# Optimization experiments

Hardware: AMD Instinct MI355X
Metric: run time of the kernel (lower is better)

The kernel has to match this reference:

```python
import jax, jax.numpy as jnp
import numpy as np

NUM_GROUPS = 32
EPS = 1e-5


def group_norm(x, scale, bias):
    # x: [B, C, L], normalize per (group, batch) over (C//G, L)
    B, C, L = x.shape
    G = NUM_GROUPS
    xg = x.reshape(B, G, C // G, L)
    mean = xg.mean(axis=(2, 3), keepdims=True)
    var = xg.var(axis=(2, 3), keepdims=True)
    xg = (xg - mean) * jax.lax.rsqrt(var + EPS)
    h = xg.reshape(B, C, L)
    return h * scale[None, :, None] + bias[None, :, None]


def setup_inputs() -> dict:
    key = jax.random.key(0)
    ks = jax.random.split(key, 8)
    B, C, L = 8, 512, 2048
    s = 1.0 / np.sqrt(C)
    return {
        "x": jax.random.normal(ks[0], (B, C, L), jnp.float32),
        "gn_scale": jnp.ones((C,), jnp.float32),
        "gn_bias": jnp.zeros((C,), jnp.float32),
        "wq": jax.random.normal(ks[1], (C, C), jnp.float32) * s,
        "bq": jnp.zeros((C,), jnp.float32),
        "wk": jax.random.normal(ks[2], (C, C), jnp.float32) * s,
        "bk": jnp.zeros((C,), jnp.float32),
        "wv": jax.random.normal(ks[3], (C, C), jnp.float32) * s,
        "bv": jnp.zeros((C,), jnp.float32),
        "wo": jax.random.normal(ks[4], (C, C), jnp.float32) * s,
        "bo": jnp.zeros((C,), jnp.float32),
    }


def reference(x, gn_scale, gn_bias, wq, bq, wk, bk, wv, bv, wo, bo):
    B, C, L = x.shape
    h = group_norm(x, gn_scale, gn_bias)  # [B, C, L]
    # 1x1 conv == per-position linear; produce [B, L, C] directly
    q = jnp.einsum('oc,bcl->blo', wq, h) + bq
    k = jnp.einsum('oc,bcl->blo', wk, h) + bk
    v = jnp.einsum('oc,bcl->blo', wv, h) + bv
    scale = jnp.asarray(C, x.dtype) ** -0.5
    w = jnp.einsum('bqc,bkc->bqk', q, k) * scale  # [B, L, L]
    w = jax.nn.softmax(w, axis=-1)
    a = jnp.einsum('bqk,bkc->bqc', w, v)  # [B, L, C]
    out = jnp.einsum('oc,blc->bol', wo, a) + bo[None, :, None]  # [B, C, L]
    return x + out
```

## Files before the change

### kernel.cpp

```cpp
#include <hip/hip_runtime.h>

typedef __attribute__((ext_vector_type(8))) _Float16 half8;
typedef __attribute__((ext_vector_type(4))) float floatx4;

#define AS1 __attribute__((address_space(1)))
#define AS3 __attribute__((address_space(3)))

__device__ __forceinline__ void async_load16(const void* g, void* l) {
  __builtin_amdgcn_global_load_lds((AS1 void*)(unsigned long long)g,
                                   (AS3 void*)(unsigned long long)l, 16, 0, 0);
}

__global__ __launch_bounds__(256) void gn_stats(const float* __restrict__ x,
                                                float* __restrict__ stats) {
  const int bg = blockIdx.x;
  const float4* p4 = (const float4*)(x + (long long)bg * 32768);
  const int t = threadIdx.x;
  float s = 0.f, ss = 0.f;
  for (int i = t; i < 8192; i += 256) {
    float4 v = p4[i];
    s += v.x + v.y + v.z + v.w;
    ss += v.x * v.x + v.y * v.y + v.z * v.z + v.w * v.w;
  }
#pragma unroll
  for (int off = 32; off; off >>= 1) { s += __shfl_down(s, off); ss += __shfl_down(ss, off); }
  __shared__ float rs[4], rss[4];
  if ((t & 63) == 0) { rs[t >> 6] = s; rss[t >> 6] = ss; }
  __syncthreads();
  if (t == 0) {
    s = rs[0] + rs[1] + rs[2] + rs[3];
    ss = rss[0] + rss[1] + rss[2] + rss[3];
    float mean = s * (1.f / 32768.f);
    float var = ss * (1.f / 32768.f) - mean * mean;
    stats[bg] = mean;
    stats[256 + bg] = rsqrtf(var + 1e-5f);
  }
}

__global__ __launch_bounds__(256) void gn_apply(const float* __restrict__ x,
                                                const float* __restrict__ stats,
                                                const float* __restrict__ gsc,
                                                const float* __restrict__ gbi,
                                                _Float16* __restrict__ ht) {
  __shared__ float tile[64][65];
  const int b = blockIdx.z, c0 = blockIdx.y * 64, l0 = blockIdx.x * 64;
  const int t = threadIdx.x, tr = t >> 6, tc = t & 63;
  const float* xb = x + ((long long)b * 512 + c0) * 2048 + l0;
#pragma unroll
  for (int p = 0; p < 16; ++p) {
    int row = tr + p * 4;
    tile[row][tc] = xb[(long long)row * 2048 + tc];
  }
  __syncthreads();
  const int c = c0 + tc;
  const int bg = b * 32 + (c >> 4);
  const float mean = stats[bg], rstd = stats[256 + bg];
  const float sc = gsc[c] * rstd;
  const float off = gbi[c] - mean * sc;
  _Float16* hb = ht + ((long long)b * 2048 + l0) * 512 + c0;
#pragma unroll
  for (int p = 0; p < 16; ++p) {
    int l = tr + p * 4;
    hb[(long long)l * 512 + tc] = (_Float16)(tile[tc][l] * sc + off);
  }
}

__global__ __launch_bounds__(256) void cast_w(const float* __restrict__ w0, const float* __restrict__ w1,
                                              const float* __restrict__ w2, const float* __restrict__ w3,
                                              const float* __restrict__ bq, const float* __restrict__ bk,
                                              _Float16* __restrict__ outw, float* __restrict__ bqk) {
  const long long i = (long long)blockIdx.x * 256 + threadIdx.x;
  if (blockIdx.x < 4096) {
    const int m = (int)(i >> 18);
    const int r = (int)(i & 262143);
    const float* w = (m == 0) ? w0 : (m == 1) ? w1 : (m == 2) ? w2 : w3;
    outw[i] = (_Float16)w[r];
  } else {
    const int j = (int)(i - 4096LL * 256);
    bqk[j] = (j < 512) ? bq[j] : bk[j - 512];
  }
}

template <int BIAS_MODE , int OUT_TYPE , bool RESIDUAL>
__global__ __launch_bounds__(256) void gemm_bt(
    const _Float16* __restrict__ A, long long sA, int lda,
    const _Float16* __restrict__ Bt, long long sB, int ldb,
    void* __restrict__ Cv, long long sC, int ldc,
    const float* __restrict__ bias,
    const float* __restrict__ resid, long long sR,
    float alpha, int K) {
  __shared__ __align__(16) _Float16 lsa[128 * 64];
  __shared__ __align__(16) _Float16 lsb[128 * 64];
  const int tid = threadIdx.x;
  const int wave = tid >> 6, lane = tid & 63;
  const int bz = blockIdx.x;
  const int m0 = blockIdx.y * 128, n0 = blockIdx.z * 128;
  A += (long long)bz * sA;
  Bt += (long long)bz * sB;

  const bool isA = (wave < 2);
  const _Float16* gsrc = isA ? A : Bt;
  const int ld = isA ? lda : ldb;
  const int rbase = (wave & 1) * 64;
  const int t0 = isA ? m0 : n0;
  _Float16* lbase = (isA ? lsa : lsb) + rbase * 64;
  const int grow = t0 + rbase + (lane >> 3);
  const int gcol = ((lane & 7) ^ ((lane >> 3) & 7)) * 8;

  floatx4 acc[4][4] = {};
  const int mw = (wave >> 1) * 64, nw = (wave & 1) * 64;
  const int fm = lane & 15;
  const int quad = lane >> 4;

  for (int k0 = 0; k0 < K; k0 += 64) {
    __syncthreads();
    const _Float16* g = gsrc + (long long)grow * ld + k0 + gcol;
#pragma unroll
    for (int s = 0; s < 8; ++s)
      async_load16(g + (long long)s * 8 * ld, lbase + s * 512);
    __syncthreads();
#pragma unroll
    for (int kk = 0; kk < 2; ++kk) {
      const int ca = quad + 4 * kk;
      const int cs = (ca ^ (fm & 7)) * 8;
      half8 af[4], bfr[4];
#pragma unroll
      for (int i = 0; i < 4; ++i) af[i] = *(const half8*)&lsa[(mw + 16 * i + fm) * 64 + cs];
#pragma unroll
      for (int j = 0; j < 4; ++j) bfr[j] = *(const half8*)&lsb[(nw + 16 * j + fm) * 64 + cs];
#pragma unroll
      for (int i = 0; i < 4; ++i)
#pragma unroll
        for (int j = 0; j < 4; ++j)
          acc[i][j] = __builtin_amdgcn_mfma_f32_16x16x32_f16(af[i], bfr[j], acc[i][j], 0, 0, 0);
    }
  }

  const int r0 = m0 + mw + quad * 4;
  const int c0 = n0 + nw + fm;
#pragma unroll
  for (int i = 0; i < 4; ++i) {
#pragma unroll
    for (int j = 0; j < 4; ++j) {
      const int cc = c0 + 16 * j;
#pragma unroll
      for (int t = 0; t < 4; ++t) {
        const int rr = r0 + 16 * i + t;
        float v = acc[i][j][t] * alpha;
        if (BIAS_MODE == 1) v += bias[cc];
        if (BIAS_MODE == 2) v += bias[rr];
        if (RESIDUAL) v += resid[(long long)bz * sR + (long long)rr * ldc + cc];
        const long long off = (long long)bz * sC + (long long)rr * ldc + cc;
        if (OUT_TYPE == 0) ((float*)Cv)[off] = v;
        else ((_Float16*)Cv)[off] = (_Float16)v;
      }
    }
  }
}

__global__ __launch_bounds__(256) void softmax_inplace(_Float16* __restrict__ S) {
  const long long row = (long long)blockIdx.y * 2048 + blockIdx.x;
  _Float16* p = S + row * 2048;
  const int t = threadIdx.x;
  union U { float4 f; _Float16 h[8]; } u;
  u.f = ((const float4*)p)[t];
  float v[8];
  float mx = -3e38f;
#pragma unroll
  for (int i = 0; i < 8; ++i) { v[i] = (float)u.h[i]; mx = fmaxf(mx, v[i]); }
#pragma unroll
  for (int off = 32; off; off >>= 1) mx = fmaxf(mx, __shfl_down(mx, off));
  __shared__ float red[4];
  if ((t & 63) == 0) red[t >> 6] = mx;
  __syncthreads();
  mx = fmaxf(fmaxf(red[0], red[1]), fmaxf(red[2], red[3]));
  float s = 0.f;
#pragma unroll
  for (int i = 0; i < 8; ++i) { v[i] = __expf(v[i] - mx); s += v[i]; }
#pragma unroll
  for (int off = 32; off; off >>= 1) s += __shfl_down(s, off);
  __syncthreads();
  if ((t & 63) == 0) red[t >> 6] = s;
  __syncthreads();
  s = red[0] + red[1] + red[2] + red[3];
  const float inv = 1.f / s;
#pragma unroll
  for (int i = 0; i < 8; ++i) u.h[i] = (_Float16)(v[i] * inv);
  ((float4*)p)[t] = u.f;
}

extern "C" void kernel_launch(void* const* d_in, const int* in_sizes, int n_in,
                              void* d_out, int out_size, void* d_ws, size_t ws_size,
                              hipStream_t stream) {
  const float* x = (const float*)d_in[0];
  const float* gsc = (const float*)d_in[1];
  const float* gbi = (const float*)d_in[2];
  const float* wq = (const float*)d_in[3];
  const float* bq = (const float*)d_in[4];
  const float* wk = (const float*)d_in[5];
  const float* bk = (const float*)d_in[6];
  const float* wv = (const float*)d_in[7];
  const float* bv = (const float*)d_in[8];
  const float* wo = (const float*)d_in[9];
  const float* bo = (const float*)d_in[10];
  float* out = (float*)d_out;

  char* ws = (char*)d_ws;
  float* stats = (float*)ws;
  float* bqk = (float*)(ws + 2048);
  _Float16* wbf = (_Float16*)(ws + 8192);
  _Float16* ht = wbf + 4 * 262144;
  const long long EB = 8LL * 2048 * 512;
  _Float16* qk = ht + EB;
  _Float16* vm = qk + 2 * EB;
  _Float16* Sb = vm + EB;
  _Float16* at = ht;

  gn_stats<<<256, 256, 0, stream>>>(x, stats);
  gn_apply<<<dim3(32, 8, 8), 256, 0, stream>>>(x, stats, gsc, gbi, ht);
  cast_w<<<4100, 256, 0, stream>>>(wq, wk, wv, wo, bq, bk, wbf, bqk);

  const float scale = 0.044194173824159216f;
  gemm_bt<1, 1, false><<<dim3(8, 16, 8), 256, 0, stream>>>(
      ht, 1048576LL, 512, wbf, 0LL, 512, qk, 2097152LL, 1024, bqk, nullptr, 0LL, 1.f, 512);
  gemm_bt<2, 1, false><<<dim3(8, 4, 16), 256, 0, stream>>>(
      wbf + 2 * 262144, 0LL, 512, ht, 1048576LL, 512, vm, 1048576LL, 2048, bv, nullptr, 0LL, 1.f, 512);
  gemm_bt<0, 1, false><<<dim3(8, 16, 16), 256, 0, stream>>>(
      qk, 2097152LL, 1024, qk + 512, 2097152LL, 1024, Sb, 4194304LL, 2048, nullptr, nullptr, 0LL, scale, 512);
  softmax_inplace<<<dim3(2048, 8), 256, 0, stream>>>(Sb);
  gemm_bt<0, 1, false><<<dim3(8, 16, 4), 256, 0, stream>>>(
      Sb, 4194304LL, 2048, vm, 1048576LL, 2048, at, 1048576LL, 512, nullptr, nullptr, 0LL, 1.f, 2048);
  gemm_bt<2, 0, true><<<dim3(8, 4, 16), 256, 0, stream>>>(
      wbf + 3 * 262144, 0LL, 512, at, 1048576LL, 512, out, 1048576LL, 2048, bo, x, 1048576LL, 1.f, 512);
}
```

Measured before the change: 288.1 us.

## Replace GEMM kernel with 8-wave double-buffered ping-pong pipelined tiles

Replaces the single-buffered 128x128 GEMM with a 512-thread kernel that uses larger 256x256 or 128x256 tiles and double-buffered LDS. Loads for the next k-tile are issued in quarter-sized stages and interleaved with MFMA quadrants, using explicit vmcnt waits, barriers and s_setprio. The goal is to hide global-to-LDS latency behind compute and raise data reuse per block. In exchange, register and LDS use per block grows, and grids become smaller, which may leave some CUs idle on the smaller GEMMs.

```diff
diff --git a/kernel.cpp b/kernel.cpp
--- a/kernel.cpp
+++ b/kernel.cpp
@@ -9,6 +9,17 @@
 __device__ __forceinline__ void async_load16(const void* g, void* l) {
   __builtin_amdgcn_global_load_lds((AS1 void*)(unsigned long long)g,
                                    (AS3 void*)(unsigned long long)l, 16, 0, 0);
+}
+
+template <int N>
+__device__ __forceinline__ void wait_vm() {
+  if constexpr (N == 0) asm volatile("s_waitcnt vmcnt(0)" ::: "memory");
+  else if constexpr (N == 1) asm volatile("s_waitcnt vmcnt(1)" ::: "memory");
+  else if constexpr (N == 2) asm volatile("s_waitcnt vmcnt(2)" ::: "memory");
+  else if constexpr (N == 3) asm volatile("s_waitcnt vmcnt(3)" ::: "memory");
+  else if constexpr (N == 4) asm volatile("s_waitcnt vmcnt(4)" ::: "memory");
+  else if constexpr (N == 5) asm volatile("s_waitcnt vmcnt(5)" ::: "memory");
+  else asm volatile("s_waitcnt vmcnt(6)" ::: "memory");
 }
 
 __global__ __launch_bounds__(256) void gn_stats(const float* __restrict__ x,
@@ -81,81 +92,170 @@
   }
 }
 
-template <int BIAS_MODE , int OUT_TYPE , bool RESIDUAL>
-__global__ __launch_bounds__(256) void gemm_bt(
+template <int BM, int BN, int BIAS_MODE , int OUT_TYPE , bool RESIDUAL>
+__global__ __launch_bounds__(512, 2) void gemm8p(
     const _Float16* __restrict__ A, long long sA, int lda,
     const _Float16* __restrict__ Bt, long long sB, int ldb,
     void* __restrict__ Cv, long long sC, int ldc,
     const float* __restrict__ bias,
     const float* __restrict__ resid, long long sR,
     float alpha, int K) {
-  __shared__ __align__(16) _Float16 lsa[128 * 64];
-  __shared__ __align__(16) _Float16 lsb[128 * 64];
+  constexpr int ASZ = BM * 64, BSZ = BN * 64;
+  constexpr int BUF = ASZ + BSZ;
+  constexpr int RWA = BM / 16, RWB = BN / 16;
+  constexpr int LA = RWA / 8, LB = RWB / 8;
+  constexpr int NMI = BM / 64, NNJ = BN / 128;
+  __shared__ __align__(16) _Float16 ls[2 * BUF];
+
   const int tid = threadIdx.x;
   const int wave = tid >> 6, lane = tid & 63;
+  const int wr = wave >> 2, wc = wave & 3;
+  const int fm = lane & 15, q = lane >> 4;
   const int bz = blockIdx.x;
-  const int m0 = blockIdx.y * 128, n0 = blockIdx.z * 128;
+  const int m0 = blockIdx.y * BM, n0 = blockIdx.z * BN;
   A += (long long)bz * sA;
   Bt += (long long)bz * sB;
 
-  const bool isA = (wave < 2);
-  const _Float16* gsrc = isA ? A : Bt;
-  const int ld = isA ? lda : ldb;
-  const int rbase = (wave & 1) * 64;
-  const int t0 = isA ? m0 : n0;
-  _Float16* lbase = (isA ? lsa : lsb) + rbase * 64;
-  const int grow = t0 + rbase + (lane >> 3);
-  const int gcol = ((lane & 7) ^ ((lane >> 3) & 7)) * 8;
-
-  floatx4 acc[4][4] = {};
-  const int mw = (wave >> 1) * 64, nw = (wave & 1) * 64;
-  const int fm = lane & 15;
-  const int quad = lane >> 4;
-
-  for (int k0 = 0; k0 < K; k0 += 64) {
-    __syncthreads();
-    const _Float16* g = gsrc + (long long)grow * ld + k0 + gcol;
-#pragma unroll
-    for (int s = 0; s < 8; ++s)
-      async_load16(g + (long long)s * 8 * ld, lbase + s * 512);
-    __syncthreads();
-#pragma unroll
-    for (int kk = 0; kk < 2; ++kk) {
-      const int ca = quad + 4 * kk;
-      const int cs = (ca ^ (fm & 7)) * 8;
-      half8 af[4], bfr[4];
-#pragma unroll
-      for (int i = 0; i < 4; ++i) af[i] = *(const half8*)&lsa[(mw + 16 * i + fm) * 64 + cs];
-#pragma unroll
-      for (int j = 0; j < 4; ++j) bfr[j] = *(const half8*)&lsb[(nw + 16 * j + fm) * 64 + cs];
-#pragma unroll
-      for (int i = 0; i < 4; ++i)
-#pragma unroll
-        for (int j = 0; j < 4; ++j)
-          acc[i][j] = __builtin_amdgcn_mfma_f32_16x16x32_f16(af[i], bfr[j], acc[i][j], 0, 0, 0);
-    }
-  }
-
-  const int r0 = m0 + mw + quad * 4;
-  const int c0 = n0 + nw + fm;
-#pragma unroll
-  for (int i = 0; i < 4; ++i) {
-#pragma unroll
-    for (int j = 0; j < 4; ++j) {
-      const int cc = c0 + 16 * j;
-#pragma unroll
-      for (int t = 0; t < 4; ++t) {
-        const int rr = r0 + 16 * i + t;
-        float v = acc[i][j][t] * alpha;
-        if (BIAS_MODE == 1) v += bias[cc];
-        if (BIAS_MODE == 2) v += bias[rr];
-        if (RESIDUAL) v += resid[(long long)bz * sR + (long long)rr * ldc + cc];
-        const long long off = (long long)bz * sC + (long long)rr * ldc + cc;
-        if (OUT_TYPE == 0) ((float*)Cv)[off] = v;
-        else ((_Float16*)Cv)[off] = (_Float16)v;
-      }
-    }
-  }
+  const int srow = lane >> 3;
+  const int schunk = ((lane & 7) ^ (srow & 7)) * 8;
+  const _Float16* pA0 = A + (long long)(m0 + RWA * wave + srow) * lda + schunk;
+  const _Float16* pA1 = pA0 + (long long)(BM / 2) * lda;
+  const _Float16* pB0 = Bt + (long long)(n0 + RWB * wave + srow) * ldb + schunk;
+  const _Float16* pB1 = pB0 + (long long)(BN / 2) * ldb;
+  const int dA0 = RWA * wave * 64;
+  const int dB0 = ASZ + RWB * wave * 64;
+
+  const int c0 = (q ^ (fm & 7)) * 8;
+  const int c1 = ((q + 4) ^ (fm & 7)) * 8;
+  const int arow = wr * (BM / 4) + fm;
+  const int brow = wc * (BN / 8) + fm;
+
+  floatx4 acc[2][2][NMI][NNJ] = {};
+  half8 af[NMI][2], bf0[NNJ][2], bf1[NNJ][2];
+
+  const int NT = K >> 6;
+
+  {
+    _Float16* st = ls;
+#pragma unroll
+    for (int s = 0; s < LA; ++s) async_load16(pA0 + (long long)(8 * s) * lda, st + dA0 + s * 512);
+#pragma unroll
+    for (int s = 0; s < LB; ++s) async_load16(pB0 + (long long)(8 * s) * ldb, st + dB0 + s * 512);
+#pragma unroll
+    for (int s = 0; s < LB; ++s) async_load16(pB1 + (long long)(8 * s) * ldb, st + dB0 + BSZ / 2 + s * 512);
+#pragma unroll
+    for (int s = 0; s < LA; ++s) async_load16(pA1 + (long long)(8 * s) * lda, st + dA0 + ASZ / 2 + s * 512);
+    pA0 += 64; pA1 += 64; pB0 += 64; pB1 += 64;
+    wait_vm<0>();
+    __builtin_amdgcn_s_barrier();
+  }
+
+#define G8_READ_A(MH)                                                      \
+  _Pragma("unroll") for (int mi = 0; mi < NMI; ++mi) {                     \
+    const int r_ = (MH) * (BM / 2) + arow + 16 * mi;                       \
+    af[mi][0] = *(const half8*)&cb[r_ * 64 + c0];                          \
+    af[mi][1] = *(const half8*)&cb[r_ * 64 + c1];                          \
+  }
+#define G8_READ_B(NH, BF)                                                  \
+  _Pragma("unroll") for (int nj = 0; nj < NNJ; ++nj) {                     \
+    const int r_ = ASZ + ((NH) * (BN / 2) + brow + 16 * nj) * 64;          \
+    BF[nj][0] = *(const half8*)&cb[r_ + c0];                               \
+    BF[nj][1] = *(const half8*)&cb[r_ + c1];                               \
+  }
+#define G8_MFMA(MH, NH, BF)                                                \
+  __builtin_amdgcn_s_setprio(1);                                           \
+  _Pragma("unroll") for (int mi = 0; mi < NMI; ++mi)                       \
+  _Pragma("unroll") for (int nj = 0; nj < NNJ; ++nj) {                     \
+    acc[MH][NH][mi][nj] = __builtin_amdgcn_mfma_f32_16x16x32_f16(          \
+        af[mi][0], BF[nj][0], acc[MH][NH][mi][nj], 0, 0, 0);               \
+    acc[MH][NH][mi][nj] = __builtin_amdgcn_mfma_f32_16x16x32_f16(          \
+        af[mi][1], BF[nj][1], acc[MH][NH][mi][nj], 0, 0, 0);               \
+  }                                                                        \
+  __builtin_amdgcn_s_setprio(0);
+#define G8_STAGE_A(PTR, OFF)                                               \
+  _Pragma("unroll") for (int s = 0; s < LA; ++s)                           \
+    async_load16(PTR + (long long)(8 * s) * lda, st + dA0 + (OFF) + s * 512);
+#define G8_STAGE_B(PTR, OFF)                                               \
+  _Pragma("unroll") for (int s = 0; s < LB; ++s)                           \
+    async_load16(PTR + (long long)(8 * s) * ldb, st + dB0 + (OFF) + s * 512);
+
+  for (int kt = 0; kt < NT - 1; ++kt) {
+    const _Float16* cb = ls + (kt & 1) * BUF;
+    _Float16* st = ls + ((kt + 1) & 1) * BUF;
+    G8_READ_A(0)
+    G8_READ_B(0, bf0)
+    G8_STAGE_A(pA0, 0)
+    wait_vm<2 * LA>();
+    __builtin_amdgcn_s_barrier();
+    G8_MFMA(0, 0, bf0)
+    __builtin_amdgcn_s_barrier();
+    G8_READ_B(1, bf1)
+    G8_STAGE_B(pB0, 0)
+    wait_vm<LA + LB>();
+    __builtin_amdgcn_s_barrier();
+    G8_MFMA(0, 1, bf1)
+    __builtin_amdgcn_s_barrier();
+    G8_READ_A(1)
+    G8_STAGE_B(pB1, BSZ / 2)
+    wait_vm<2 * LB>();
+    __builtin_amdgcn_s_barrier();
+    G8_MFMA(1, 1, bf1)
+    __builtin_amdgcn_s_barrier();
+    G8_STAGE_A(pA1, ASZ / 2)
+    wait_vm<LA + LB>();
+    __builtin_amdgcn_s_barrier();
+    G8_MFMA(1, 0, bf0)
+    __builtin_amdgcn_s_barrier();
+    pA0 += 64; pA1 += 64; pB0 += 64; pB1 += 64;
+  }
+  {
+    const _Float16* cb = ls + ((NT - 1) & 1) * BUF;
+    G8_READ_A(0)
+    G8_READ_B(0, bf0)
+    wait_vm<LA>();
+    __builtin_amdgcn_s_barrier();
+    G8_MFMA(0, 0, bf0)
+    __builtin_amdgcn_s_barrier();
+    G8_READ_B(1, bf1)
+    wait_vm<0>();
+    __builtin_amdgcn_s_barrier();
+    G8_MFMA(0, 1, bf1)
+    __builtin_amdgcn_s_barrier();
+    G8_READ_A(1)
+    __builtin_amdgcn_s_barrier();
+    G8_MFMA(1, 1, bf1)
+    __builtin_amdgcn_s_barrier();
+    G8_MFMA(1, 0, bf0)
+  }
+
+#undef G8_READ_A
+#undef G8_READ_B
+#undef G8_MFMA
+#undef G8_STAGE_A
+#undef G8_STAGE_B
+
+#pragma unroll
+  for (int mh = 0; mh < 2; ++mh)
+#pragma unroll
+    for (int nh = 0; nh < 2; ++nh)
+#pragma unroll
+      for (int mi = 0; mi < NMI; ++mi)
+#pragma unroll
+        for (int nj = 0; nj < NNJ; ++nj) {
+          const int rr0 = m0 + mh * (BM / 2) + wr * (BM / 4) + 16 * mi + 4 * q;
+          const int cc = n0 + nh * (BN / 2) + wc * (BN / 8) + 16 * nj + fm;
+#pragma unroll
+          for (int t = 0; t < 4; ++t) {
+            const int rr = rr0 + t;
+            float v = acc[mh][nh][mi][nj][t] * alpha;
+            if (BIAS_MODE == 1) v += bias[cc];
+            if (BIAS_MODE == 2) v += bias[rr];
+            if (RESIDUAL) v += resid[(long long)bz * sR + (long long)rr * ldc + cc];
+            const long long off = (long long)bz * sC + (long long)rr * ldc + cc;
+            if (OUT_TYPE == 0) ((float*)Cv)[off] = v;
+            else ((_Float16*)Cv)[off] = (_Float16)v;
+          }
+        }
 }
 
 __global__ __launch_bounds__(256) void softmax_inplace(_Float16* __restrict__ S) {
@@ -221,15 +321,15 @@
   cast_w<<<4100, 256, 0, stream>>>(wq, wk, wv, wo, bq, bk, wbf, bqk);
 
   const float scale = 0.044194173824159216f;
-  gemm_bt<1, 1, false><<<dim3(8, 16, 8), 256, 0, stream>>>(
+  gemm8p<256, 256, 1, 1, false><<<dim3(8, 8, 4), 512, 0, stream>>>(
       ht, 1048576LL, 512, wbf, 0LL, 512, qk, 2097152LL, 1024, bqk, nullptr, 0LL, 1.f, 512);
-  gemm_bt<2, 1, false><<<dim3(8, 4, 16), 256, 0, stream>>>(
+  gemm8p<128, 256, 2, 1, false><<<dim3(8, 4, 8), 512, 0, stream>>>(
       wbf + 2 * 262144, 0LL, 512, ht, 1048576LL, 512, vm, 1048576LL, 2048, bv, nullptr, 0LL, 1.f, 512);
-  gemm_bt<0, 1, false><<<dim3(8, 16, 16), 256, 0, stream>>>(
+  gemm8p<256, 256, 0, 1, false><<<dim3(8, 8, 8), 512, 0, stream>>>(
       qk, 2097152LL, 1024, qk + 512, 2097152LL, 1024, Sb, 4194304LL, 2048, nullptr, nullptr, 0LL, scale, 512);
   softmax_inplace<<<dim3(2048, 8), 256, 0, stream>>>(Sb);
-  gemm_bt<0, 1, false><<<dim3(8, 16, 4), 256, 0, stream>>>(
+  gemm8p<128, 256, 0, 1, false><<<dim3(8, 16, 2), 512, 0, stream>>>(
       Sb, 4194304LL, 2048, vm, 1048576LL, 2048, at, 1048576LL, 512, nullptr, nullptr, 0LL, 1.f, 2048);
-  gemm_bt<2, 0, true><<<dim3(8, 4, 16), 256, 0, stream>>>(
+  gemm8p<128, 256, 2, 0, true><<<dim3(8, 4, 8), 512, 0, stream>>>(
       wbf + 3 * 262144, 0LL, 512, at, 1048576LL, 512, out, 1048576LL, 2048, bo, x, 1048576LL, 1.f, 512);
 }
```

Result: no change. 282.8 us (-1.8%).
